# Optimization experiments

Hardware: AMD Instinct MI355X
Metric: run time of the kernel (lower is better)

Reference implementation:

```python
import jax, jax.numpy as jnp
import numpy as np

TEMPERATURE = 0.5
BATCH_SIZE = 4096
EPS = 1e-8  # torch.nn.CosineSimilarity default eps


def setup_inputs() -> dict:
    key = jax.random.key(0)
    k1, k2 = jax.random.split(key)
    z1 = jax.random.normal(k1, (BATCH_SIZE, 256), dtype=jnp.float32)
    z2 = jax.random.normal(k2, (BATCH_SIZE, 256), dtype=jnp.float32)
    return {"z1": z1, "z2": z2}


def reference(z1, z2):
    B = z1.shape[0]
    N = 2 * B
    reps = jnp.concatenate([z1, z2], axis=0)  # [N, D]
    # Cosine similarity (torch clamps each norm to eps before dividing)
    norms = jnp.maximum(jnp.linalg.norm(reps, axis=1, keepdims=True), EPS)
    z = reps / norms
    sim = z @ z.T  # [N, N] cosine similarity matrix

    # positives: diagonals at offsets +B and -B (they are identical by symmetry,
    # but keep the original concat order: [diag(+B), diag(-B)])
    l_pos = jnp.diagonal(sim, offset=B)
    r_pos = jnp.diagonal(sim, offset=-B)
    positives = jnp.concatenate([l_pos, r_pos])  # [N]

    inv_t = 1.0 / TEMPERATURE
    pos_logit = positives * inv_t  # logits[:, 0]

    # negatives are all off-diagonal entries of each row (the positive pair is
    # thus present twice in the logits, faithful to the original). CE with
    # label 0 => loss_i = logsumexp(logits_i) - logits_i[0].
    neg_logits = jnp.where(jnp.eye(N, dtype=bool), -jnp.inf, sim * inv_t)
    lse = jnp.logaddexp(pos_logit, jax.scipy.special.logsumexp(neg_logits, axis=1))
    loss = jnp.sum(lse - pos_logit) / N
    return loss
```

## Files before the change

### kernel.cpp

```cpp
#include <hip/hip_runtime.h>
#include <hip/hip_bf16.h>
#include <cstdint>
#include <cstddef>
#include <math.h>

#define BSZ   4096
#define NROW  8192
#define DIM   256
#define INV_T 2.0f
#define EPS_N 1e-8f

typedef __attribute__((ext_vector_type(4))) float f32x4;

__device__ __forceinline__ void load_lds16(const void* g, void* l) {
    __builtin_amdgcn_global_load_lds(
        (const __attribute__((address_space(1))) void*)g,
        (__attribute__((address_space(3))) void*)l,
        16, 0, 0);
}

__global__ __launch_bounds__(256)
void nt_normalize(const float* __restrict__ z1,
                  const float* __restrict__ z2,
                  char* __restrict__ zn3,
                  unsigned int* __restrict__ cnt) {
    const int wave = threadIdx.x >> 6;
    const int lane = threadIdx.x & 63;
    const int row  = blockIdx.x * 4 + wave;
    const float* src = (row < BSZ) ? (z1 + (size_t)row * DIM)
                                   : (z2 + (size_t)(row - BSZ) * DIM);
    const float4 v = ((const float4*)src)[lane];
    float ss = v.x * v.x + v.y * v.y + v.z * v.z + v.w * v.w;
    #pragma unroll
    for (int off = 32; off; off >>= 1) ss += __shfl_xor(ss, off);
    const float rinv = 1.0f / fmaxf(sqrtf(ss), EPS_N);
    int pk = 0;
    pk = __builtin_amdgcn_cvt_pk_fp8_f32(v.x * rinv, v.y * rinv, pk, false);
    pk = __builtin_amdgcn_cvt_pk_fp8_f32(v.z * rinv, v.w * rinv, pk, true);
    const int s    = row >> 7;
    const int lrow = row & 127;
    const int kc   = lane >> 4;
    const int unit = (lane >> 1) & 7;
    const int off4 = (lane & 1) * 4;
    const int u    = unit ^ (lrow & 7);
    *(int*)(zn3 + (size_t)s * 32768 + kc * 8192 + lrow * 64 + u * 8 + off4) = pk;
    if (row == 0 && lane == 0) *cnt = 0;
}

__global__ __launch_bounds__(256)
void nt_gram(const char* __restrict__ zn3,
             float* __restrict__ part,
             float* __restrict__ pos) {
    const int l = blockIdx.x;
    int bi = (int)((129.0 - sqrt(16641.0 - 8.0 * (double)l)) * 0.5);
    while (64 * (bi + 1) - (bi + 1) * bi / 2 <= l) ++bi;
    while (64 * bi - bi * (bi - 1) / 2 > l) --bi;
    const int bj = bi + (l - (64 * bi - bi * (bi - 1) / 2));

    __shared__ char As[8192];
    __shared__ char Bs[8192];

    const int t    = threadIdx.x;
    const int lane = t & 63;
    const int wave = t >> 6;
    const int wrow = (wave >> 1) * 64;
    const int wcol = (wave & 1) * 64;
    const int q    = lane >> 4;
    const int r16  = lane & 15;
    const int sw   = r16 & 7;
    const int t16  = t * 16;

    const char* A2 = zn3 + (size_t)bi * 32768;
    const char* B2 = zn3 + (size_t)bj * 32768;

    f32x4 acc[4][4] = {};

    for (int kc = 0; kc < 4; ++kc) {
        load_lds16(A2 + kc * 8192 + t16,        As + t16);
        load_lds16(A2 + kc * 8192 + 4096 + t16, As + 4096 + t16);
        load_lds16(B2 + kc * 8192 + t16,        Bs + t16);
        load_lds16(B2 + kc * 8192 + 4096 + t16, Bs + 4096 + t16);
        __syncthreads();

        #pragma unroll
        for (int kh = 0; kh < 2; ++kh) {
            const int spos = (((kh << 2) + q) ^ sw) << 3;
            long af[4], bfv[4];
            #pragma unroll
            for (int mi = 0; mi < 4; ++mi)
                af[mi] = *(const long*)(As + (wrow + mi * 16 + r16) * 64 + spos);
            #pragma unroll
            for (int ni = 0; ni < 4; ++ni)
                bfv[ni] = *(const long*)(Bs + (wcol + ni * 16 + r16) * 64 + spos);
            #pragma unroll
            for (int mi = 0; mi < 4; ++mi)
                #pragma unroll
                for (int ni = 0; ni < 4; ++ni)
                    acc[mi][ni] = __builtin_amdgcn_mfma_f32_16x16x32_fp8_fp8(
                        af[mi], bfv[ni], acc[mi][ni], 0, 0, 0);
        }
        __syncthreads();
    }

    const int c = r16;
    const bool diag_block = (bi == bj);
    const int rslot = 2 * bj + (wcol >> 6);
    const int cslot = 2 * bi + (wrow >> 6);
    float colp[4] = {0.f, 0.f, 0.f, 0.f};

    #pragma unroll
    for (int mi = 0; mi < 4; ++mi) {
        #pragma unroll
        for (int r = 0; r < 4; ++r) {
            const int grow = bi * 128 + wrow + mi * 16 + q * 4 + r;
            float s = 0.f;
            #pragma unroll
            for (int ni = 0; ni < 4; ++ni) {
                const int gcol = bj * 128 + wcol + ni * 16 + c;
                const float val = acc[mi][ni][r];
                float e = __expf(val * INV_T);
                e = (grow == gcol) ? 0.f : e;
                s += e;
                colp[ni] += e;
                if (gcol == grow + BSZ) {
                    pos[grow] = val;
                    pos[gcol] = val;
                }
            }
            s += __shfl_xor(s, 1);
            s += __shfl_xor(s, 2);
            s += __shfl_xor(s, 4);
            s += __shfl_xor(s, 8);
            if (c == 0) part[(size_t)grow * 128 + rslot] = s;
        }
    }
    if (!diag_block) {
        #pragma unroll
        for (int ni = 0; ni < 4; ++ni) {
            float cs = colp[ni];
            cs += __shfl_xor(cs, 16);
            cs += __shfl_xor(cs, 32);
            if (q == 0)
                part[(size_t)(bj * 128 + wcol + ni * 16 + c) * 128 + cslot] = cs;
        }
    }
}

__global__ __launch_bounds__(256)
void nt_finalize(const float* __restrict__ part,
                 const float* __restrict__ pos,
                 float* __restrict__ blocksum,
                 unsigned int* __restrict__ cnt,
                 float* __restrict__ out) {
    const int b    = blockIdx.x;
    const int t    = threadIdx.x;
    const int lane = t & 63;
    const int row  = b * 128 + (t >> 1);
    const int half = t & 1;

    const float4* p4 = (const float4*)(part + (size_t)row * 128 + half * 64);
    float s = 0.f;
    #pragma unroll
    for (int j = 0; j < 16; ++j) {
        const float4 v = p4[j];
        s += v.x + v.y + v.z + v.w;
    }
    s += __shfl_xor(s, 1);
    float contrib = 0.f;
    if (half == 0) {
        const float pl = pos[row] * INV_T;
        contrib = logf(__expf(pl) + s) - pl;
    }
    #pragma unroll
    for (int off = 32; off; off >>= 1) contrib += __shfl_xor(contrib, off);
    __shared__ float r4[4];
    __shared__ int   slast;
    if (lane == 0) r4[t >> 6] = contrib;
    __syncthreads();
    if (t == 0) {
        blocksum[b] = r4[0] + r4[1] + r4[2] + r4[3];
        __threadfence();
        slast = (atomicAdd(cnt, 1u) == 63u);
    }
    __syncthreads();
    if (slast && t < 64) {
        float v = atomicAdd(&blocksum[t], 0.0f);
        #pragma unroll
        for (int off = 32; off; off >>= 1) v += __shfl_xor(v, off);
        if (t == 0) out[0] = v * (1.0f / NROW);
    }
}

extern "C" void kernel_launch(void* const* d_in, const int* in_sizes, int n_in,
                              void* d_out, int out_size, void* d_ws, size_t ws_size,
                              hipStream_t stream) {
    const float* z1 = (const float*)d_in[0];
    const float* z2 = (const float*)d_in[1];
    float* out = (float*)d_out;

    char*  zn3      = (char*)d_ws;
    float* part     = (float*)((char*)d_ws + (size_t)2097152);
    float* pos      = (float*)((char*)d_ws + (size_t)6291456);
    float* blocksum = pos + NROW;
    unsigned int* cnt = (unsigned int*)(blocksum + 64);

    nt_normalize<<<NROW / 4, 256, 0, stream>>>(z1, z2, zn3, cnt);
    nt_gram<<<2080, 256, 0, stream>>>(zn3, part, pos);
    nt_finalize<<<64, 256, 0, stream>>>(part, pos, blocksum, cnt, out);
}
```

Measured before the change: 94.79 us.

## Double-buffer LDS tiles in gram kernel to overlap loads with MFMA

Replaces the single-buffered K loop in the gram kernel with a manually unrolled two-stage pipeline over a 32KB LDS buffer. The next K chunk is issued with global_load_lds while the current chunk is computed, using explicit vmcnt waits and raw s_barrier instead of __syncthreads. The aim is to hide global-to-LDS latency behind MFMA work. In exchange, LDS use per block doubles, which may lower occupancy. The hand-placed waits and barriers are also fragile to get correct.

```diff
diff --git a/kernel.cpp b/kernel.cpp
--- a/kernel.cpp
+++ b/kernel.cpp
@@ -18,6 +18,8 @@
         (__attribute__((address_space(3))) void*)l,
         16, 0, 0);
 }
+
+#define VMWAIT(N) asm volatile("s_waitcnt vmcnt(" #N ")" ::: "memory")
 
 __global__ __launch_bounds__(256)
 void nt_normalize(const float* __restrict__ z1,
@@ -57,8 +59,7 @@
     while (64 * bi - bi * (bi - 1) / 2 > l) --bi;
     const int bj = bi + (l - (64 * bi - bi * (bi - 1) / 2));
 
-    __shared__ char As[8192];
-    __shared__ char Bs[8192];
+    __shared__ char lds[32768];
 
     const int t    = threadIdx.x;
     const int lane = t & 63;
@@ -75,32 +76,60 @@
 
     f32x4 acc[4][4] = {};
 
-    for (int kc = 0; kc < 4; ++kc) {
-        load_lds16(A2 + kc * 8192 + t16,        As + t16);
-        load_lds16(A2 + kc * 8192 + 4096 + t16, As + 4096 + t16);
-        load_lds16(B2 + kc * 8192 + t16,        Bs + t16);
-        load_lds16(B2 + kc * 8192 + 4096 + t16, Bs + 4096 + t16);
-        __syncthreads();
-
-        #pragma unroll
-        for (int kh = 0; kh < 2; ++kh) {
-            const int spos = (((kh << 2) + q) ^ sw) << 3;
-            long af[4], bfv[4];
-            #pragma unroll
-            for (int mi = 0; mi < 4; ++mi)
-                af[mi] = *(const long*)(As + (wrow + mi * 16 + r16) * 64 + spos);
-            #pragma unroll
-            for (int ni = 0; ni < 4; ++ni)
-                bfv[ni] = *(const long*)(Bs + (wcol + ni * 16 + r16) * 64 + spos);
-            #pragma unroll
-            for (int mi = 0; mi < 4; ++mi)
-                #pragma unroll
-                for (int ni = 0; ni < 4; ++ni)
-                    acc[mi][ni] = __builtin_amdgcn_mfma_f32_16x16x32_fp8_fp8(
-                        af[mi], bfv[ni], acc[mi][ni], 0, 0, 0);
-        }
-        __syncthreads();
-    }
+#define STAGE(kc, buf)                                                   \
+    {                                                                    \
+        char* d_ = lds + (buf) * 16384;                                  \
+        load_lds16(A2 + (kc) * 8192 + t16,        d_ + t16);             \
+        load_lds16(A2 + (kc) * 8192 + 4096 + t16, d_ + 4096 + t16);      \
+        load_lds16(B2 + (kc) * 8192 + t16,        d_ + 8192 + t16);      \
+        load_lds16(B2 + (kc) * 8192 + 4096 + t16, d_ + 12288 + t16);     \
+    }
+
+#define COMPUTE(buf)                                                     \
+    {                                                                    \
+        const char* As_ = lds + (buf) * 16384;                           \
+        const char* Bs_ = As_ + 8192;                                    \
+        _Pragma("unroll")                                                \
+        for (int kh = 0; kh < 2; ++kh) {                                 \
+            const int spos = (((kh << 2) + q) ^ sw) << 3;                \
+            long af[4], bfv[4];                                          \
+            _Pragma("unroll")                                            \
+            for (int mi = 0; mi < 4; ++mi)                               \
+                af[mi] = *(const long*)(As_ + (wrow + mi * 16 + r16) * 64 + spos); \
+            _Pragma("unroll")                                            \
+            for (int ni = 0; ni < 4; ++ni)                               \
+                bfv[ni] = *(const long*)(Bs_ + (wcol + ni * 16 + r16) * 64 + spos); \
+            _Pragma("unroll")                                            \
+            for (int mi = 0; mi < 4; ++mi)                               \
+                _Pragma("unroll")                                        \
+                for (int ni = 0; ni < 4; ++ni)                           \
+                    acc[mi][ni] = __builtin_amdgcn_mfma_f32_16x16x32_fp8_fp8( \
+                        af[mi], bfv[ni], acc[mi][ni], 0, 0, 0);          \
+        }                                                                \
+    }
+
+    STAGE(0, 0)
+    STAGE(1, 1)
+    VMWAIT(4);
+    __builtin_amdgcn_s_barrier();
+    COMPUTE(0)
+    __builtin_amdgcn_s_barrier();
+    __builtin_amdgcn_sched_barrier(0);
+    STAGE(2, 0)
+    VMWAIT(4);
+    __builtin_amdgcn_s_barrier();
+    COMPUTE(1)
+    __builtin_amdgcn_s_barrier();
+    __builtin_amdgcn_sched_barrier(0);
+    STAGE(3, 1)
+    VMWAIT(4);
+    __builtin_amdgcn_s_barrier();
+    COMPUTE(0)
+    VMWAIT(0);
+    __builtin_amdgcn_s_barrier();
+    COMPUTE(1)
+#undef STAGE
+#undef COMPUTE
 
     const int c = r16;
     const bool diag_block = (bi == bj);
```

Result: no change. 95.07 us (median of 2 runs) (+0.3%).
